# Performance work log

Measured on AMD Instinct MI355X. Metric: run time of the kernel, lower is better.

The kernel has to match this reference:

```python
import jax, jax.numpy as jnp
import numpy as np


def setup_inputs() -> dict:
    key = jax.random.key(0)
    k1, k2 = jax.random.split(key)
    B, F = 256, 512
    mu_in = jax.random.normal(k1, (B, F), dtype=jnp.float32)
    Sigma_in = jax.random.normal(k2, (B, F, F), dtype=jnp.float32)
    return {"mu_in": mu_in, "Sigma_in": Sigma_in}


def reference(mu_in, Sigma_in):
    # mu_out = softmax(mu_in, axis=1)
    p = jax.nn.softmax(mu_in, axis=1)  # [B, F]
    # Per-sample softmax Jacobian J = diag(p) - p p^T (closed form of the
    # autograd.functional.jacobian block-diagonal the torch code extracts).
    # Sigma_out = J @ Sigma_in @ J^T, computed without materializing J:
    #   (Sigma J^T)_ij = p_j * (Sigma_ij - (Sigma @ p)_i)
    Sp = jnp.einsum("bij,bj->bi", Sigma_in, p)  # [B, F]
    M = p[:, None, :] * (Sigma_in - Sp[:, :, None])  # Sigma @ J^T, [B, F, F]
    #   (J M)_ik = p_i * (M_ik - (p^T M)_k)
    pM = jnp.einsum("bi,bik->bk", p, M)  # [B, F]
    Sigma_out = p[:, :, None] * (M - pM[:, None, :])  # [B, F, F]
    return (p, Sigma_out)
```

## Files before the change

kernel.cpp:

```cpp
#include <hip/hip_runtime.h>

#define FDIM 512
#define S_ELEMS (FDIM * FDIM)

#define R_OFF      0
#define C_OFF      131072
#define S_OFF      262144
#define CP_OFF     262400
#define WS_FLOATS  (262400 + 256 * 8 * 512)

__device__ __forceinline__ float4 ld4(const float* p) { return *(const float4*)p; }

typedef float vf4 __attribute__((ext_vector_type(4)));
__device__ __forceinline__ void st4nt(float* p, float4 v) {
    __builtin_nontemporal_store(*(vf4*)&v, (vf4*)p);
}

__global__ __launch_bounds__(256)
void k1_rc(const float* __restrict__ mu,
           const float* __restrict__ Sigma,
           float* __restrict__ p_out,
           float* __restrict__ ws) {
    const int bid  = blockIdx.x;
    const int b    = bid >> 3;
    const int slab = bid & 7;
    const int t = threadIdx.x;
    const int w = t >> 6;
    const int l = t & 63;

    __shared__ __align__(16) float p_lds[FDIM];
    __shared__ __align__(16) float cred[4][FDIM];
    __shared__ float red[4];
    __shared__ float sc[1];

    const float x0 = mu[(size_t)b * FDIM + t];
    const float x1 = mu[(size_t)b * FDIM + t + 256];
    float m = fmaxf(x0, x1);
    #pragma unroll
    for (int off = 32; off >= 1; off >>= 1) m = fmaxf(m, __shfl_xor(m, off));
    if (l == 0) red[w] = m;
    __syncthreads();
    if (t == 0) sc[0] = fmaxf(fmaxf(red[0], red[1]), fmaxf(red[2], red[3]));
    __syncthreads();
    const float mx = sc[0];
    const float e0 = __expf(x0 - mx);
    const float e1 = __expf(x1 - mx);
    float ssum = e0 + e1;
    #pragma unroll
    for (int off = 32; off >= 1; off >>= 1) ssum += __shfl_xor(ssum, off);
    if (l == 0) red[w] = ssum;
    __syncthreads();
    if (t == 0) sc[0] = red[0] + red[1] + red[2] + red[3];
    __syncthreads();
    const float inv = 1.0f / sc[0];
    const float pva = e0 * inv, pvb = e1 * inv;
    p_lds[t] = pva;
    p_lds[t + 256] = pvb;
    if (slab == 0) {
        p_out[(size_t)b * FDIM + t] = pva;
        p_out[(size_t)b * FDIM + t + 256] = pvb;
    }
    __syncthreads();

    const float4 p0 = ld4(&p_lds[4 * l]);
    const float4 p1 = ld4(&p_lds[256 + 4 * l]);

    const int i0 = slab * 64 + w * 16;
    const float* base = Sigma + (size_t)b * S_ELEMS + (size_t)i0 * FDIM + 4 * l;
    float* r_ws = ws + R_OFF + (size_t)b * FDIM;

    float4 c0 = make_float4(0.f, 0.f, 0.f, 0.f);
    float4 c1 = make_float4(0.f, 0.f, 0.f, 0.f);
    float4 A0, A1, B0, B1, C0, C1, D0, D1;

#define LD1(P, q) do { const float* gp_ = base + (size_t)(q) * FDIM;        \
    P##0 = ld4(gp_); P##1 = ld4(gp_ + 256); } while (0)

#define RCROW(v0, v1, q) do {                                               \
    const int i_ = i0 + (q);                                                \
    float dot = v0.x*p0.x + v0.y*p0.y + v0.z*p0.z + v0.w*p0.w               \
              + v1.x*p1.x + v1.y*p1.y + v1.z*p1.z + v1.w*p1.w;              \
    _Pragma("unroll")                                                       \
    for (int o_ = 32; o_ >= 1; o_ >>= 1) dot += __shfl_xor(dot, o_);        \
    if (l == 0) r_ws[i_] = dot;                                             \
    const float pi_ = p_lds[i_];                                            \
    c0.x += pi_*v0.x; c0.y += pi_*v0.y; c0.z += pi_*v0.z; c0.w += pi_*v0.w; \
    c1.x += pi_*v1.x; c1.y += pi_*v1.y; c1.z += pi_*v1.z; c1.w += pi_*v1.w; \
} while (0)
#define RC1(P, q) RCROW(P##0, P##1, q)

    LD1(A, 0); LD1(B, 1); LD1(C, 2);
    RC1(A, 0);  LD1(D, 3);
    RC1(B, 1);  LD1(A, 4);
    RC1(C, 2);  LD1(B, 5);
    RC1(D, 3);  LD1(C, 6);
    RC1(A, 4);  LD1(D, 7);
    RC1(B, 5);  LD1(A, 8);
    RC1(C, 6);  LD1(B, 9);
    RC1(D, 7);  LD1(C, 10);
    RC1(A, 8);  LD1(D, 11);
    RC1(B, 9);  LD1(A, 12);
    RC1(C, 10); LD1(B, 13);
    RC1(D, 11); LD1(C, 14);
    RC1(A, 12); LD1(D, 15);
    RC1(B, 13);
    RC1(C, 14);
    RC1(D, 15);
#undef LD1
#undef RCROW
#undef RC1

    *(float4*)&cred[w][4 * l] = c0;
    *(float4*)&cred[w][256 + 4 * l] = c1;
    __syncthreads();
    const float ca = cred[0][t] + cred[1][t] + cred[2][t] + cred[3][t];
    const float cb = cred[0][t + 256] + cred[1][t + 256] + cred[2][t + 256] + cred[3][t + 256];
    float* cp = ws + CP_OFF + ((size_t)b * 8 + slab) * FDIM;
    cp[t] = ca;
    cp[t + 256] = cb;
}

__global__ __launch_bounds__(512)
void k2b_cs(const float* __restrict__ p_out, float* __restrict__ ws) {
    const int b = blockIdx.x;
    const int t = threadIdx.x;
    const int w = t >> 6;
    const int l = t & 63;
    __shared__ float red[8];

    float cc = 0.f;
    #pragma unroll
    for (int j = 0; j < 8; ++j)
        cc += ws[CP_OFF + ((size_t)b * 8 + j) * FDIM + t];
    ws[C_OFF + (size_t)b * FDIM + t] = cc;

    float sv = p_out[(size_t)b * FDIM + t] * ws[R_OFF + (size_t)b * FDIM + t];
    #pragma unroll
    for (int off = 32; off >= 1; off >>= 1) sv += __shfl_xor(sv, off);
    if (l == 0) red[w] = sv;
    __syncthreads();
    if (t == 0) {
        float tt = 0.f;
        for (int j = 0; j < 8; ++j) tt += red[j];
        ws[S_OFF + b] = tt;
    }
}

__global__ __launch_bounds__(256)
void k3_out(const float* __restrict__ Sigma,
            const float* __restrict__ p_out,
            const float* __restrict__ ws,
            float* __restrict__ S_out) {
    const int bid  = 2047 - (int)blockIdx.x;
    const int b    = bid >> 3;
    const int slab = bid & 7;
    const int t = threadIdx.x;
    const int w = t >> 6;
    const int l = t & 63;

    __shared__ float pr[64], rr[64];
    if (t < 64) {
        pr[t] = p_out[(size_t)b * FDIM + slab * 64 + t];
        rr[t] = ws[R_OFF + (size_t)b * FDIM + slab * 64 + t];
    }
    const float4 p0 = ld4(p_out + (size_t)b * FDIM + 4 * l);
    const float4 p1 = ld4(p_out + (size_t)b * FDIM + 256 + 4 * l);
    const float4 c0 = ld4(ws + C_OFF + (size_t)b * FDIM + 4 * l);
    const float4 c1 = ld4(ws + C_OFF + (size_t)b * FDIM + 256 + 4 * l);
    const float  s  = ws[S_OFF + b];
    __syncthreads();

    const int i0 = slab * 64 + w * 16;
    const float* base = Sigma + (size_t)b * S_ELEMS + (size_t)i0 * FDIM + 4 * l;
    float* obase      = S_out + (size_t)b * S_ELEMS + (size_t)i0 * FDIM + 4 * l;

    float4 A0, A1, B0, B1, C0, C1, D0, D1;

#define LD3(P, q) do { const float* gp_ = base + (size_t)(q) * FDIM;        \
    P##0 = ld4(gp_); P##1 = ld4(gp_ + 256); } while (0)

#define OWROW(v0, v1, q) do {                                               \
    const int lr_ = w * 16 + (q);                                           \
    const float pi_ = pr[lr_];                                              \
    const float f_  = s - rr[lr_];                                          \
    float4 o0, o1;                                                          \
    o0.x = pi_*p0.x*(v0.x + (f_ - c0.x));                                   \
    o0.y = pi_*p0.y*(v0.y + (f_ - c0.y));                                   \
    o0.z = pi_*p0.z*(v0.z + (f_ - c0.z));                                   \
    o0.w = pi_*p0.w*(v0.w + (f_ - c0.w));                                   \
    o1.x = pi_*p1.x*(v1.x + (f_ - c1.x));                                   \
    o1.y = pi_*p1.y*(v1.y + (f_ - c1.y));                                   \
    o1.z = pi_*p1.z*(v1.z + (f_ - c1.z));                                   \
    o1.w = pi_*p1.w*(v1.w + (f_ - c1.w));                                   \
    float* op_ = obase + (size_t)(q) * FDIM;                                \
    st4nt(op_, o0); st4nt(op_ + 256, o1);                                   \
} while (0)
#define OW3(P, q) OWROW(P##0, P##1, q)

    LD3(A, 0); LD3(B, 1); LD3(C, 2);
    OW3(A, 0);  LD3(D, 3);
    OW3(B, 1);  LD3(A, 4);
    OW3(C, 2);  LD3(B, 5);
    OW3(D, 3);  LD3(C, 6);
    OW3(A, 4);  LD3(D, 7);
    OW3(B, 5);  LD3(A, 8);
    OW3(C, 6);  LD3(B, 9);
    OW3(D, 7);  LD3(C, 10);
    OW3(A, 8);  LD3(D, 11);
    OW3(B, 9);  LD3(A, 12);
    OW3(C, 10); LD3(B, 13);
    OW3(D, 11); LD3(C, 14);
    OW3(A, 12); LD3(D, 15);
    OW3(B, 13);
    OW3(C, 14);
    OW3(D, 15);
#undef LD3
#undef OWROW
#undef OW3
}

__global__ __launch_bounds__(1024, 1)
void rvsoftmax_fused(const float* __restrict__ mu,
                     const float* __restrict__ Sigma,
                     float* __restrict__ p_out,
                     float* __restrict__ S_out) {
    const int b = blockIdx.x, t = threadIdx.x, w = t >> 6, l = t & 63;
    __shared__ __align__(16) float p_lds[FDIM];
    __shared__ __align__(16) float r_lds[FDIM];
    __shared__ __align__(16) float c_lds[FDIM];
    __shared__ __align__(16) float c_stage[16][FDIM];
    __shared__ float red[16]; __shared__ float sc[2];
    float x = (t < FDIM) ? mu[(size_t)b * FDIM + t] : -__builtin_inff();
    float m = x;
    #pragma unroll
    for (int off = 32; off >= 1; off >>= 1) m = fmaxf(m, __shfl_xor(m, off));
    if (l == 0) red[w] = m;
    __syncthreads();
    if (t == 0) { float mm = red[0]; for (int j = 1; j < 16; ++j) mm = fmaxf(mm, red[j]); sc[0] = mm; }
    __syncthreads();
    const float mx = sc[0];
    float e = (t < FDIM) ? __expf(x - mx) : 0.f;
    float ssum = e;
    #pragma unroll
    for (int off = 32; off >= 1; off >>= 1) ssum += __shfl_xor(ssum, off);
    if (l == 0) red[w] = ssum;
    __syncthreads();
    if (t == 0) { float tt = 0.f; for (int j = 0; j < 16; ++j) tt += red[j]; sc[0] = tt; }
    __syncthreads();
    const float inv = 1.0f / sc[0];
    if (t < FDIM) { float pv = e * inv; p_lds[t] = pv; p_out[(size_t)b * FDIM + t] = pv; }
    __syncthreads();
    const float* Sb = Sigma + (size_t)b * S_ELEMS;
    const float4 p0 = ld4(&p_lds[4 * l]);
    const float4 p1 = ld4(&p_lds[256 + 4 * l]);
    float4 c0 = make_float4(0.f, 0.f, 0.f, 0.f), c1 = make_float4(0.f, 0.f, 0.f, 0.f);
    for (int j = 0; j < 32; ++j) {
        const int i = j * 16 + w;
        const float* row = Sb + (size_t)i * FDIM;
        const float4 a0 = ld4(&row[4 * l]); const float4 a1 = ld4(&row[256 + 4 * l]);
        const float pi = p_lds[i];
        float dot = a0.x*p0.x + a0.y*p0.y + a0.z*p0.z + a0.w*p0.w
                  + a1.x*p1.x + a1.y*p1.y + a1.z*p1.z + a1.w*p1.w;
        #pragma unroll
        for (int off = 32; off >= 1; off >>= 1) dot += __shfl_xor(dot, off);
        if (l == 0) r_lds[i] = dot;
        c0.x += pi*a0.x; c0.y += pi*a0.y; c0.z += pi*a0.z; c0.w += pi*a0.w;
        c1.x += pi*a1.x; c1.y += pi*a1.y; c1.z += pi*a1.z; c1.w += pi*a1.w;
    }
    *(float4*)&c_stage[w][4 * l] = c0;
    *(float4*)&c_stage[w][256 + 4 * l] = c1;
    __syncthreads();
    if (t < FDIM) {
        float cc = 0.f;
        #pragma unroll
        for (int j = 0; j < 16; ++j) cc += c_stage[j][t];
        c_lds[t] = cc;
    }
    __syncthreads();
    float sv = (t < FDIM) ? p_lds[t] * r_lds[t] : 0.f;
    #pragma unroll
    for (int off = 32; off >= 1; off >>= 1) sv += __shfl_xor(sv, off);
    if (l == 0) red[w] = sv;
    __syncthreads();
    if (t == 0) { float tt = 0.f; for (int j = 0; j < 16; ++j) tt += red[j]; sc[1] = tt; }
    __syncthreads();
    const float s = sc[1];
    const float4 cc0 = ld4(&c_lds[4 * l]); const float4 cc1 = ld4(&c_lds[256 + 4 * l]);
    float* Ob = S_out + (size_t)b * S_ELEMS;
    for (int j = 31; j >= 0; --j) {
        const int i = j * 16 + w;
        const float* row = Sb + (size_t)i * FDIM;
        float* orow = Ob + (size_t)i * FDIM;
        const float4 a0 = ld4(&row[4 * l]); const float4 a1 = ld4(&row[256 + 4 * l]);
        const float pi = p_lds[i];
        const float f = s - r_lds[i];
        float4 o0, o1;
        o0.x = pi*p0.x*(a0.x + (f - cc0.x)); o0.y = pi*p0.y*(a0.y + (f - cc0.y));
        o0.z = pi*p0.z*(a0.z + (f - cc0.z)); o0.w = pi*p0.w*(a0.w + (f - cc0.w));
        o1.x = pi*p1.x*(a1.x + (f - cc1.x)); o1.y = pi*p1.y*(a1.y + (f - cc1.y));
        o1.z = pi*p1.z*(a1.z + (f - cc1.z)); o1.w = pi*p1.w*(a1.w + (f - cc1.w));
        *(float4*)&orow[4 * l] = o0;
        *(float4*)&orow[256 + 4 * l] = o1;
    }
}

extern "C" void kernel_launch(void* const* d_in, const int* in_sizes, int n_in,
                              void* d_out, int out_size, void* d_ws, size_t ws_size,
                              hipStream_t stream) {
    (void)in_sizes; (void)n_in; (void)out_size;
    const float* mu    = (const float*)d_in[0];
    const float* Sigma = (const float*)d_in[1];
    float* p_out = (float*)d_out;
    float* S_out = (float*)d_out + (size_t)256 * FDIM;

    if (ws_size >= (size_t)WS_FLOATS * sizeof(float)) {
        float* ws = (float*)d_ws;
        hipLaunchKernelGGL(k1_rc,   dim3(2048), dim3(256), 0, stream, mu, Sigma, p_out, ws);
        hipLaunchKernelGGL(k2b_cs,  dim3(256),  dim3(512), 0, stream, p_out, ws);
        hipLaunchKernelGGL(k3_out,  dim3(2048), dim3(256), 0, stream, Sigma, p_out, ws, S_out);
    } else {
        hipLaunchKernelGGL(rvsoftmax_fused, dim3(256), dim3(1024), 0, stream,
                           mu, Sigma, p_out, S_out);
    }
}
```

Measured before the change: 136.9 us.

## Split batch into groups so Sigma stays cache-resident between passes; fold reduction kernel

```diff
diff --git a/kernel.cpp b/kernel.cpp
--- a/kernel.cpp
+++ b/kernel.cpp
@@ -2,12 +2,13 @@
 
 #define FDIM 512
 #define S_ELEMS (FDIM * FDIM)
+#define NB 256
+#define GROUPS 4
+#define BPG (NB / GROUPS)
 
 #define R_OFF      0
-#define C_OFF      131072
-#define S_OFF      262144
-#define CP_OFF     262400
-#define WS_FLOATS  (262400 + 256 * 8 * 512)
+#define CP_OFF     (NB * FDIM)
+#define WS_FLOATS  (NB * FDIM + NB * 8 * FDIM)
 
 __device__ __forceinline__ float4 ld4(const float* p) { return *(const float4*)p; }
 
@@ -20,9 +21,10 @@
 void k1_rc(const float* __restrict__ mu,
            const float* __restrict__ Sigma,
            float* __restrict__ p_out,
-           float* __restrict__ ws) {
+           float* __restrict__ ws,
+           int b0) {
     const int bid  = blockIdx.x;
-    const int b    = bid >> 3;
+    const int b    = b0 + (bid >> 3);
     const int slab = bid & 7;
     const int t = threadIdx.x;
     const int w = t >> 6;
@@ -120,55 +122,23 @@
     cp[t + 256] = cb;
 }
 
-__global__ __launch_bounds__(512)
-void k2b_cs(const float* __restrict__ p_out, float* __restrict__ ws) {
-    const int b = blockIdx.x;
-    const int t = threadIdx.x;
-    const int w = t >> 6;
-    const int l = t & 63;
-    __shared__ float red[8];
-
-    float cc = 0.f;
-    #pragma unroll
-    for (int j = 0; j < 8; ++j)
-        cc += ws[CP_OFF + ((size_t)b * 8 + j) * FDIM + t];
-    ws[C_OFF + (size_t)b * FDIM + t] = cc;
-
-    float sv = p_out[(size_t)b * FDIM + t] * ws[R_OFF + (size_t)b * FDIM + t];
-    #pragma unroll
-    for (int off = 32; off >= 1; off >>= 1) sv += __shfl_xor(sv, off);
-    if (l == 0) red[w] = sv;
-    __syncthreads();
-    if (t == 0) {
-        float tt = 0.f;
-        for (int j = 0; j < 8; ++j) tt += red[j];
-        ws[S_OFF + b] = tt;
-    }
-}
-
 __global__ __launch_bounds__(256)
 void k3_out(const float* __restrict__ Sigma,
             const float* __restrict__ p_out,
             const float* __restrict__ ws,
-            float* __restrict__ S_out) {
-    const int bid  = 2047 - (int)blockIdx.x;
-    const int b    = bid >> 3;
+            float* __restrict__ S_out,
+            int b0) {
+    const int bid  = 511 - (int)blockIdx.x;
+    const int b    = b0 + (bid >> 3);
     const int slab = bid & 7;
     const int t = threadIdx.x;
     const int w = t >> 6;
     const int l = t & 63;
 
+    __shared__ __align__(16) float c_lds[FDIM];
     __shared__ float pr[64], rr[64];
-    if (t < 64) {
-        pr[t] = p_out[(size_t)b * FDIM + slab * 64 + t];
-        rr[t] = ws[R_OFF + (size_t)b * FDIM + slab * 64 + t];
-    }
-    const float4 p0 = ld4(p_out + (size_t)b * FDIM + 4 * l);
-    const float4 p1 = ld4(p_out + (size_t)b * FDIM + 256 + 4 * l);
-    const float4 c0 = ld4(ws + C_OFF + (size_t)b * FDIM + 4 * l);
-    const float4 c1 = ld4(ws + C_OFF + (size_t)b * FDIM + 256 + 4 * l);
-    const float  s  = ws[S_OFF + b];
-    __syncthreads();
+    __shared__ float red[4];
+    __shared__ float s_sh;
 
     const int i0 = slab * 64 + w * 16;
     const float* base = Sigma + (size_t)b * S_ELEMS + (size_t)i0 * FDIM + 4 * l;
@@ -178,6 +148,39 @@
 
 #define LD3(P, q) do { const float* gp_ = base + (size_t)(q) * FDIM;        \
     P##0 = ld4(gp_); P##1 = ld4(gp_ + 256); } while (0)
+
+    LD3(A, 0); LD3(B, 1); LD3(C, 2);
+
+    const float* cp = ws + CP_OFF + (size_t)b * 8 * FDIM;
+    float ca = 0.f, cb = 0.f;
+    #pragma unroll
+    for (int j = 0; j < 8; ++j) {
+        ca += cp[(size_t)j * FDIM + t];
+        cb += cp[(size_t)j * FDIM + t + 256];
+    }
+    c_lds[t] = ca;
+    c_lds[t + 256] = cb;
+
+    const float* pb_g = p_out + (size_t)b * FDIM;
+    const float* rb_g = ws + R_OFF + (size_t)b * FDIM;
+    const float pv0 = pb_g[t], pv1 = pb_g[t + 256];
+    const float rv0 = rb_g[t], rv1 = rb_g[t + 256];
+    float sv = pv0 * rv0 + pv1 * rv1;
+    #pragma unroll
+    for (int off = 32; off >= 1; off >>= 1) sv += __shfl_xor(sv, off);
+    if (l == 0) red[w] = sv;
+    if (t < 64) {
+        pr[t] = pb_g[slab * 64 + t];
+        rr[t] = rb_g[slab * 64 + t];
+    }
+    __syncthreads();
+    if (t == 0) s_sh = red[0] + red[1] + red[2] + red[3];
+    __syncthreads();
+    const float s = s_sh;
+    const float4 p0 = ld4(pb_g + 4 * l);
+    const float4 p1 = ld4(pb_g + 256 + 4 * l);
+    const float4 c0 = ld4(&c_lds[4 * l]);
+    const float4 c1 = ld4(&c_lds[256 + 4 * l]);
 
 #define OWROW(v0, v1, q) do {                                               \
     const int lr_ = w * 16 + (q);                                           \
@@ -197,7 +200,6 @@
 } while (0)
 #define OW3(P, q) OWROW(P##0, P##1, q)
 
-    LD3(A, 0); LD3(B, 1); LD3(C, 2);
     OW3(A, 0);  LD3(D, 3);
     OW3(B, 1);  LD3(A, 4);
     OW3(C, 2);  LD3(B, 5);
@@ -311,15 +313,18 @@
     const float* mu    = (const float*)d_in[0];
     const float* Sigma = (const float*)d_in[1];
     float* p_out = (float*)d_out;
-    float* S_out = (float*)d_out + (size_t)256 * FDIM;
+    float* S_out = (float*)d_out + (size_t)NB * FDIM;
 
     if (ws_size >= (size_t)WS_FLOATS * sizeof(float)) {
         float* ws = (float*)d_ws;
-        hipLaunchKernelGGL(k1_rc,   dim3(2048), dim3(256), 0, stream, mu, Sigma, p_out, ws);
-        hipLaunchKernelGGL(k2b_cs,  dim3(256),  dim3(512), 0, stream, p_out, ws);
-        hipLaunchKernelGGL(k3_out,  dim3(2048), dim3(256), 0, stream, Sigma, p_out, ws, S_out);
+        for (int g = 0; g < GROUPS; ++g) {
+            hipLaunchKernelGGL(k1_rc,  dim3(BPG * 8), dim3(256), 0, stream,
+                               mu, Sigma, p_out, ws, g * BPG);
+            hipLaunchKernelGGL(k3_out, dim3(BPG * 8), dim3(256), 0, stream,
+                               Sigma, p_out, ws, S_out, g * BPG);
+        }
     } else {
-        hipLaunchKernelGGL(rvsoftmax_fused, dim3(256), dim3(1024), 0, stream,
+        hipLaunchKernelGGL(rvsoftmax_fused, dim3(NB), dim3(1024), 0, stream,
                            mu, Sigma, p_out, S_out);
     }
 }
```

Result: slower. 149.9 us (+9.4%).

## Split batch into groups for cache reuse of Sigma between passes

Applied to the files above, without the earlier changes.

```diff
diff --git a/kernel.cpp b/kernel.cpp
--- a/kernel.cpp
+++ b/kernel.cpp
@@ -2,12 +2,17 @@
 
 #define FDIM 512
 #define S_ELEMS (FDIM * FDIM)
-
-#define R_OFF      0
-#define C_OFF      131072
-#define S_OFF      262144
-#define CP_OFF     262400
-#define WS_FLOATS  (262400 + 256 * 8 * 512)
+#define NB 256
+#define GROUPS 2
+#define BPG (NB / GROUPS)
+#define SLABS 16
+#define GBLK (BPG * SLABS)
+
+#define R_OFF  0
+#define C_OFF  (NB * FDIM)
+#define S_OFF  (2 * NB * FDIM)
+#define CP_OFF (2 * NB * FDIM + NB)
+#define WS_FLOATS (CP_OFF + NB * SLABS * FDIM)
 
 __device__ __forceinline__ float4 ld4(const float* p) { return *(const float4*)p; }
 
@@ -17,13 +22,14 @@
 }
 
 __global__ __launch_bounds__(256)
-void k1_rc(const float* __restrict__ mu,
-           const float* __restrict__ Sigma,
-           float* __restrict__ p_out,
-           float* __restrict__ ws) {
+void k1_kernel(const float* __restrict__ mu,
+               const float* __restrict__ Sigma,
+               float* __restrict__ p_out,
+               float* __restrict__ ws,
+               int b0) {
     const int bid  = blockIdx.x;
-    const int b    = bid >> 3;
-    const int slab = bid & 7;
+    const int b    = b0 + (bid >> 4);
+    const int slab = bid & 15;
     const int t = threadIdx.x;
     const int w = t >> 6;
     const int l = t & 63;
@@ -31,7 +37,7 @@
     __shared__ __align__(16) float p_lds[FDIM];
     __shared__ __align__(16) float cred[4][FDIM];
     __shared__ float red[4];
-    __shared__ float sc[1];
+    __shared__ float sc1;
 
     const float x0 = mu[(size_t)b * FDIM + t];
     const float x1 = mu[(size_t)b * FDIM + t + 256];
@@ -40,9 +46,9 @@
     for (int off = 32; off >= 1; off >>= 1) m = fmaxf(m, __shfl_xor(m, off));
     if (l == 0) red[w] = m;
     __syncthreads();
-    if (t == 0) sc[0] = fmaxf(fmaxf(red[0], red[1]), fmaxf(red[2], red[3]));
-    __syncthreads();
-    const float mx = sc[0];
+    if (t == 0) sc1 = fmaxf(fmaxf(red[0], red[1]), fmaxf(red[2], red[3]));
+    __syncthreads();
+    const float mx = sc1;
     const float e0 = __expf(x0 - mx);
     const float e1 = __expf(x1 - mx);
     float ssum = e0 + e1;
@@ -50,9 +56,9 @@
     for (int off = 32; off >= 1; off >>= 1) ssum += __shfl_xor(ssum, off);
     if (l == 0) red[w] = ssum;
     __syncthreads();
-    if (t == 0) sc[0] = red[0] + red[1] + red[2] + red[3];
-    __syncthreads();
-    const float inv = 1.0f / sc[0];
+    if (t == 0) sc1 = red[0] + red[1] + red[2] + red[3];
+    __syncthreads();
+    const float inv = 1.0f / sc1;
     const float pva = e0 * inv, pvb = e1 * inv;
     p_lds[t] = pva;
     p_lds[t + 256] = pvb;
@@ -65,7 +71,7 @@
     const float4 p0 = ld4(&p_lds[4 * l]);
     const float4 p1 = ld4(&p_lds[256 + 4 * l]);
 
-    const int i0 = slab * 64 + w * 16;
+    const int i0 = slab * 32 + w * 8;
     const float* base = Sigma + (size_t)b * S_ELEMS + (size_t)i0 * FDIM + 4 * l;
     float* r_ws = ws + R_OFF + (size_t)b * FDIM;
 
@@ -90,22 +96,14 @@
 #define RC1(P, q) RCROW(P##0, P##1, q)
 
     LD1(A, 0); LD1(B, 1); LD1(C, 2);
-    RC1(A, 0);  LD1(D, 3);
-    RC1(B, 1);  LD1(A, 4);
-    RC1(C, 2);  LD1(B, 5);
-    RC1(D, 3);  LD1(C, 6);
-    RC1(A, 4);  LD1(D, 7);
-    RC1(B, 5);  LD1(A, 8);
-    RC1(C, 6);  LD1(B, 9);
-    RC1(D, 7);  LD1(C, 10);
-    RC1(A, 8);  LD1(D, 11);
-    RC1(B, 9);  LD1(A, 12);
-    RC1(C, 10); LD1(B, 13);
-    RC1(D, 11); LD1(C, 14);
-    RC1(A, 12); LD1(D, 15);
-    RC1(B, 13);
-    RC1(C, 14);
-    RC1(D, 15);
+    RC1(A, 0); LD1(D, 3);
+    RC1(B, 1); LD1(A, 4);
+    RC1(C, 2); LD1(B, 5);
+    RC1(D, 3); LD1(C, 6);
+    RC1(A, 4); LD1(D, 7);
+    RC1(B, 5);
+    RC1(C, 6);
+    RC1(D, 7);
 #undef LD1
 #undef RCROW
 #undef RC1
@@ -115,14 +113,14 @@
     __syncthreads();
     const float ca = cred[0][t] + cred[1][t] + cred[2][t] + cred[3][t];
     const float cb = cred[0][t + 256] + cred[1][t + 256] + cred[2][t + 256] + cred[3][t + 256];
-    float* cp = ws + CP_OFF + ((size_t)b * 8 + slab) * FDIM;
+    float* cp = ws + CP_OFF + ((size_t)b * SLABS + slab) * FDIM;
     cp[t] = ca;
     cp[t + 256] = cb;
 }
 
 __global__ __launch_bounds__(512)
-void k2b_cs(const float* __restrict__ p_out, float* __restrict__ ws) {
-    const int b = blockIdx.x;
+void k2b_kernel(const float* __restrict__ p_out, float* __restrict__ ws, int b0) {
+    const int b = b0 + (int)blockIdx.x;
     const int t = threadIdx.x;
     const int w = t >> 6;
     const int l = t & 63;
@@ -130,8 +128,8 @@
 
     float cc = 0.f;
     #pragma unroll
-    for (int j = 0; j < 8; ++j)
-        cc += ws[CP_OFF + ((size_t)b * 8 + j) * FDIM + t];
+    for (int j = 0; j < SLABS; ++j)
+        cc += ws[CP_OFF + ((size_t)b * SLABS + j) * FDIM + t];
     ws[C_OFF + (size_t)b * FDIM + t] = cc;
 
     float sv = p_out[(size_t)b * FDIM + t] * ws[R_OFF + (size_t)b * FDIM + t];
@@ -147,40 +145,46 @@
 }
 
 __global__ __launch_bounds__(256)
-void k3_out(const float* __restrict__ Sigma,
-            const float* __restrict__ p_out,
-            const float* __restrict__ ws,
-            float* __restrict__ S_out) {
-    const int bid  = 2047 - (int)blockIdx.x;
-    const int b    = bid >> 3;
-    const int slab = bid & 7;
+void k3_kernel(const float* __restrict__ Sigma,
+               const float* __restrict__ p_out,
+               const float* __restrict__ ws,
+               float* __restrict__ S_out,
+               int b0) {
+    const int bid  = (int)gridDim.x - 1 - (int)blockIdx.x;
+    const int b    = b0 + (bid >> 4);
+    const int slab = bid & 15;
     const int t = threadIdx.x;
     const int w = t >> 6;
     const int l = t & 63;
 
-    __shared__ float pr[64], rr[64];
-    if (t < 64) {
-        pr[t] = p_out[(size_t)b * FDIM + slab * 64 + t];
-        rr[t] = ws[R_OFF + (size_t)b * FDIM + slab * 64 + t];
-    }
-    const float4 p0 = ld4(p_out + (size_t)b * FDIM + 4 * l);
-    const float4 p1 = ld4(p_out + (size_t)b * FDIM + 256 + 4 * l);
+    __shared__ float pr[32], rr[32];
+
+    const int i0 = slab * 32 + w * 8;
+    const float* base = Sigma + (size_t)b * S_ELEMS + (size_t)i0 * FDIM + 4 * l;
+    float* obase      = S_out + (size_t)b * S_ELEMS + (size_t)i0 * FDIM + 4 * l;
+
+    float4 A0, A1, B0, B1, C0, C1, D0, D1;
+
+#define LD3(P, q) do { const float* gp_ = base + (size_t)(q) * FDIM;        \
+    P##0 = ld4(gp_); P##1 = ld4(gp_ + 256); } while (0)
+
+    LD3(A, 0); LD3(B, 1); LD3(C, 2);
+
+    const float* pb_g = p_out + (size_t)b * FDIM;
+    const float* rb_g = ws + R_OFF + (size_t)b * FDIM;
+    if (t < 32) {
+        pr[t] = pb_g[slab * 32 + t];
+        rr[t] = rb_g[slab * 32 + t];
+    }
+    const float  s  = ws[S_OFF + b];
+    const float4 p0 = ld4(pb_g + 4 * l);
+    const float4 p1 = ld4(pb_g + 256 + 4 * l);
     const float4 c0 = ld4(ws + C_OFF + (size_t)b * FDIM + 4 * l);
     const float4 c1 = ld4(ws + C_OFF + (size_t)b * FDIM + 256 + 4 * l);
-    const float  s  = ws[S_OFF + b];
-    __syncthreads();
-
-    const int i0 = slab * 64 + w * 16;
-    const float* base = Sigma + (size_t)b * S_ELEMS + (size_t)i0 * FDIM + 4 * l;
-    float* obase      = S_out + (size_t)b * S_ELEMS + (size_t)i0 * FDIM + 4 * l;
-
-    float4 A0, A1, B0, B1, C0, C1, D0, D1;
-
-#define LD3(P, q) do { const float* gp_ = base + (size_t)(q) * FDIM;        \
-    P##0 = ld4(gp_); P##1 = ld4(gp_ + 256); } while (0)
+    __syncthreads();
 
 #define OWROW(v0, v1, q) do {                                               \
-    const int lr_ = w * 16 + (q);                                           \
+    const int lr_ = w * 8 + (q);                                            \
     const float pi_ = pr[lr_];                                              \
     const float f_  = s - rr[lr_];                                          \
     float4 o0, o1;                                                          \
@@ -197,23 +201,14 @@
 } while (0)
 #define OW3(P, q) OWROW(P##0, P##1, q)
 
-    LD3(A, 0); LD3(B, 1); LD3(C, 2);
-    OW3(A, 0);  LD3(D, 3);
-    OW3(B, 1);  LD3(A, 4);
-    OW3(C, 2);  LD3(B, 5);
-    OW3(D, 3);  LD3(C, 6);
-    OW3(A, 4);  LD3(D, 7);
-    OW3(B, 5);  LD3(A, 8);
-    OW3(C, 6);  LD3(B, 9);
-    OW3(D, 7);  LD3(C, 10);
-    OW3(A, 8);  LD3(D, 11);
-    OW3(B, 9);  LD3(A, 12);
-    OW3(C, 10); LD3(B, 13);
-    OW3(D, 11); LD3(C, 14);
-    OW3(A, 12); LD3(D, 15);
-    OW3(B, 13);
-    OW3(C, 14);
-    OW3(D, 15);
+    OW3(A, 0); LD3(D, 3);
+    OW3(B, 1); LD3(A, 4);
+    OW3(C, 2); LD3(B, 5);
+    OW3(D, 3); LD3(C, 6);
+    OW3(A, 4); LD3(D, 7);
+    OW3(B, 5);
+    OW3(C, 6);
+    OW3(D, 7);
 #undef LD3
 #undef OWROW
 #undef OW3
@@ -311,15 +306,21 @@
     const float* mu    = (const float*)d_in[0];
     const float* Sigma = (const float*)d_in[1];
     float* p_out = (float*)d_out;
-    float* S_out = (float*)d_out + (size_t)256 * FDIM;
+    float* S_out = (float*)d_out + (size_t)NB * FDIM;
 
     if (ws_size >= (size_t)WS_FLOATS * sizeof(float)) {
         float* ws = (float*)d_ws;
-        hipLaunchKernelGGL(k1_rc,   dim3(2048), dim3(256), 0, stream, mu, Sigma, p_out, ws);
-        hipLaunchKernelGGL(k2b_cs,  dim3(256),  dim3(512), 0, stream, p_out, ws);
-        hipLaunchKernelGGL(k3_out,  dim3(2048), dim3(256), 0, stream, Sigma, p_out, ws, S_out);
+        for (int g = 0; g < GROUPS; ++g) {
+            const int b0 = g * BPG;
+            hipLaunchKernelGGL(k1_kernel,  dim3(GBLK), dim3(256), 0, stream,
+                               mu, Sigma, p_out, ws, b0);
+            hipLaunchKernelGGL(k2b_kernel, dim3(BPG),  dim3(512), 0, stream,
+                               p_out, ws, b0);
+            hipLaunchKernelGGL(k3_kernel,  dim3(GBLK), dim3(256), 0, stream,
+                               Sigma, p_out, ws, S_out, b0);
+        }
     } else {
-        hipLaunchKernelGGL(rvsoftmax_fused, dim3(256), dim3(1024), 0, stream,
+        hipLaunchKernelGGL(rvsoftmax_fused, dim3(NB), dim3(1024), 0, stream,
                            mu, Sigma, p_out, S_out);
     }
 }
```

Measured after the change: 144.6 us. +5.6%, slower.

## Cache Sigma as fp16 in workspace during first pass and read it in output pass

Applied to the files above, without the earlier changes.

```diff
diff --git a/kernel.cpp b/kernel.cpp
--- a/kernel.cpp
+++ b/kernel.cpp
@@ -1,26 +1,43 @@
 #include <hip/hip_runtime.h>
+#include <hip/hip_fp16.h>
 
 #define FDIM 512
 #define S_ELEMS (FDIM * FDIM)
-
-#define R_OFF      0
-#define C_OFF      131072
-#define S_OFF      262144
-#define CP_OFF     262400
-#define WS_FLOATS  (262400 + 256 * 8 * 512)
+#define NB 256
+#define SLABS 8
+#define NBLK (NB * SLABS)
+
+#define R_OFF  0
+#define C_OFF  131072
+#define S_OFF  262144
+#define CP_OFF 262400
+#define H_OFF  (CP_OFF + NB * SLABS * FDIM)
+#define WS_FLOATS (H_OFF + NB * S_ELEMS / 2)
 
 __device__ __forceinline__ float4 ld4(const float* p) { return *(const float4*)p; }
 
 typedef float vf4 __attribute__((ext_vector_type(4)));
+__device__ __forceinline__ float4 ld4nt(const float* p) {
+    vf4 v = __builtin_nontemporal_load((const vf4*)p);
+    return *(float4*)&v;
+}
 __device__ __forceinline__ void st4nt(float* p, float4 v) {
     __builtin_nontemporal_store(*(vf4*)&v, (vf4*)p);
 }
+__device__ __forceinline__ unsigned pk2(float a, float b) {
+    __half2 h = __floats2half2_rn(a, b);
+    return *reinterpret_cast<unsigned*>(&h);
+}
+__device__ __forceinline__ float2 uh2(unsigned u) {
+    __half2 h = *reinterpret_cast<__half2*>(&u);
+    return __half22float2(h);
+}
 
 __global__ __launch_bounds__(256)
-void k1_rc(const float* __restrict__ mu,
-           const float* __restrict__ Sigma,
-           float* __restrict__ p_out,
-           float* __restrict__ ws) {
+void k1_kernel(const float* __restrict__ mu,
+               const float* __restrict__ Sigma,
+               float* __restrict__ p_out,
+               float* __restrict__ ws) {
     const int bid  = blockIdx.x;
     const int b    = bid >> 3;
     const int slab = bid & 7;
@@ -31,7 +48,7 @@
     __shared__ __align__(16) float p_lds[FDIM];
     __shared__ __align__(16) float cred[4][FDIM];
     __shared__ float red[4];
-    __shared__ float sc[1];
+    __shared__ float sc1;
 
     const float x0 = mu[(size_t)b * FDIM + t];
     const float x1 = mu[(size_t)b * FDIM + t + 256];
@@ -40,9 +57,9 @@
     for (int off = 32; off >= 1; off >>= 1) m = fmaxf(m, __shfl_xor(m, off));
     if (l == 0) red[w] = m;
     __syncthreads();
-    if (t == 0) sc[0] = fmaxf(fmaxf(red[0], red[1]), fmaxf(red[2], red[3]));
-    __syncthreads();
-    const float mx = sc[0];
+    if (t == 0) sc1 = fmaxf(fmaxf(red[0], red[1]), fmaxf(red[2], red[3]));
+    __syncthreads();
+    const float mx = sc1;
     const float e0 = __expf(x0 - mx);
     const float e1 = __expf(x1 - mx);
     float ssum = e0 + e1;
@@ -50,9 +67,9 @@
     for (int off = 32; off >= 1; off >>= 1) ssum += __shfl_xor(ssum, off);
     if (l == 0) red[w] = ssum;
     __syncthreads();
-    if (t == 0) sc[0] = red[0] + red[1] + red[2] + red[3];
-    __syncthreads();
-    const float inv = 1.0f / sc[0];
+    if (t == 0) sc1 = red[0] + red[1] + red[2] + red[3];
+    __syncthreads();
+    const float inv = 1.0f / sc1;
     const float pva = e0 * inv, pvb = e1 * inv;
     p_lds[t] = pva;
     p_lds[t + 256] = pvb;
@@ -68,13 +85,15 @@
     const int i0 = slab * 64 + w * 16;
     const float* base = Sigma + (size_t)b * S_ELEMS + (size_t)i0 * FDIM + 4 * l;
     float* r_ws = ws + R_OFF + (size_t)b * FDIM;
+    __half* h_base = (__half*)(ws + H_OFF) + (size_t)b * S_ELEMS
+                   + (size_t)i0 * FDIM + 8 * l;
 
     float4 c0 = make_float4(0.f, 0.f, 0.f, 0.f);
     float4 c1 = make_float4(0.f, 0.f, 0.f, 0.f);
     float4 A0, A1, B0, B1, C0, C1, D0, D1;
 
 #define LD1(P, q) do { const float* gp_ = base + (size_t)(q) * FDIM;        \
-    P##0 = ld4(gp_); P##1 = ld4(gp_ + 256); } while (0)
+    P##0 = ld4nt(gp_); P##1 = ld4nt(gp_ + 256); } while (0)
 
 #define RCROW(v0, v1, q) do {                                               \
     const int i_ = i0 + (q);                                                \
@@ -86,6 +105,10 @@
     const float pi_ = p_lds[i_];                                            \
     c0.x += pi_*v0.x; c0.y += pi_*v0.y; c0.z += pi_*v0.z; c0.w += pi_*v0.w; \
     c1.x += pi_*v1.x; c1.y += pi_*v1.y; c1.z += pi_*v1.z; c1.w += pi_*v1.w; \
+    uint4 hu_;                                                              \
+    hu_.x = pk2(v0.x, v0.y); hu_.y = pk2(v0.z, v0.w);                       \
+    hu_.z = pk2(v1.x, v1.y); hu_.w = pk2(v1.z, v1.w);                       \
+    *(uint4*)(h_base + (size_t)(q) * FDIM) = hu_;                           \
 } while (0)
 #define RC1(P, q) RCROW(P##0, P##1, q)
 
@@ -115,13 +138,13 @@
     __syncthreads();
     const float ca = cred[0][t] + cred[1][t] + cred[2][t] + cred[3][t];
     const float cb = cred[0][t + 256] + cred[1][t + 256] + cred[2][t + 256] + cred[3][t + 256];
-    float* cp = ws + CP_OFF + ((size_t)b * 8 + slab) * FDIM;
+    float* cp = ws + CP_OFF + ((size_t)b * SLABS + slab) * FDIM;
     cp[t] = ca;
     cp[t + 256] = cb;
 }
 
 __global__ __launch_bounds__(512)
-void k2b_cs(const float* __restrict__ p_out, float* __restrict__ ws) {
+void k2b_kernel(const float* __restrict__ p_out, float* __restrict__ ws) {
     const int b = blockIdx.x;
     const int t = threadIdx.x;
     const int w = t >> 6;
@@ -130,8 +153,8 @@
 
     float cc = 0.f;
     #pragma unroll
-    for (int j = 0; j < 8; ++j)
-        cc += ws[CP_OFF + ((size_t)b * 8 + j) * FDIM + t];
+    for (int j = 0; j < SLABS; ++j)
+        cc += ws[CP_OFF + ((size_t)b * SLABS + j) * FDIM + t];
     ws[C_OFF + (size_t)b * FDIM + t] = cc;
 
     float sv = p_out[(size_t)b * FDIM + t] * ws[R_OFF + (size_t)b * FDIM + t];
@@ -147,11 +170,10 @@
 }
 
 __global__ __launch_bounds__(256)
-void k3_out(const float* __restrict__ Sigma,
-            const float* __restrict__ p_out,
-            const float* __restrict__ ws,
-            float* __restrict__ S_out) {
-    const int bid  = 2047 - (int)blockIdx.x;
+void k3_kernel(const float* __restrict__ p_out,
+               const float* __restrict__ ws,
+               float* __restrict__ S_out) {
+    const int bid  = NBLK - 1 - (int)blockIdx.x;
     const int b    = bid >> 3;
     const int slab = bid & 7;
     const int t = threadIdx.x;
@@ -159,64 +181,68 @@
     const int l = t & 63;
 
     __shared__ float pr[64], rr[64];
+
+    const int i0 = slab * 64 + w * 16;
+    const __half* hb = (const __half*)(ws + H_OFF) + (size_t)b * S_ELEMS
+                     + (size_t)i0 * FDIM + 8 * l;
+    float* obase = S_out + (size_t)b * S_ELEMS + (size_t)i0 * FDIM + 4 * l;
+
+    uint4 UA, UB, UC, UD;
+
+#define LD3(U, q) U = *(const uint4*)(hb + (size_t)(q) * FDIM)
+
+    LD3(UA, 0); LD3(UB, 1); LD3(UC, 2);
+
+    const float* pb_g = p_out + (size_t)b * FDIM;
+    const float* rb_g = ws + R_OFF + (size_t)b * FDIM;
     if (t < 64) {
-        pr[t] = p_out[(size_t)b * FDIM + slab * 64 + t];
-        rr[t] = ws[R_OFF + (size_t)b * FDIM + slab * 64 + t];
-    }
-    const float4 p0 = ld4(p_out + (size_t)b * FDIM + 4 * l);
-    const float4 p1 = ld4(p_out + (size_t)b * FDIM + 256 + 4 * l);
+        pr[t] = pb_g[slab * 64 + t];
+        rr[t] = rb_g[slab * 64 + t];
+    }
+    const float  s  = ws[S_OFF + b];
+    const float4 p0 = ld4(pb_g + 4 * l);
+    const float4 p1 = ld4(pb_g + 256 + 4 * l);
     const float4 c0 = ld4(ws + C_OFF + (size_t)b * FDIM + 4 * l);
     const float4 c1 = ld4(ws + C_OFF + (size_t)b * FDIM + 256 + 4 * l);
-    const float  s  = ws[S_OFF + b];
-    __syncthreads();
-
-    const int i0 = slab * 64 + w * 16;
-    const float* base = Sigma + (size_t)b * S_ELEMS + (size_t)i0 * FDIM + 4 * l;
-    float* obase      = S_out + (size_t)b * S_ELEMS + (size_t)i0 * FDIM + 4 * l;
-
-    float4 A0, A1, B0, B1, C0, C1, D0, D1;
-
-#define LD3(P, q) do { const float* gp_ = base + (size_t)(q) * FDIM;        \
-    P##0 = ld4(gp_); P##1 = ld4(gp_ + 256); } while (0)
-
-#define OWROW(v0, v1, q) do {                                               \
+    __syncthreads();
+
+#define OWROW(U, q) do {                                                    \
+    const float2 f0_ = uh2(U.x), f1_ = uh2(U.y);                            \
+    const float2 f2_ = uh2(U.z), f3_ = uh2(U.w);                            \
     const int lr_ = w * 16 + (q);                                           \
     const float pi_ = pr[lr_];                                              \
     const float f_  = s - rr[lr_];                                          \
     float4 o0, o1;                                                          \
-    o0.x = pi_*p0.x*(v0.x + (f_ - c0.x));                                   \
-    o0.y = pi_*p0.y*(v0.y + (f_ - c0.y));                                   \
-    o0.z = pi_*p0.z*(v0.z + (f_ - c0.z));                                   \
-    o0.w = pi_*p0.w*(v0.w + (f_ - c0.w));                                   \
-    o1.x = pi_*p1.x*(v1.x + (f_ - c1.x));                                   \
-    o1.y = pi_*p1.y*(v1.y + (f_ - c1.y));                                   \
-    o1.z = pi_*p1.z*(v1.z + (f_ - c1.z));                                   \
-    o1.w = pi_*p1.w*(v1.w + (f_ - c1.w));                                   \
+    o0.x = pi_*p0.x*(f0_.x + (f_ - c0.x));                                  \
+    o0.y = pi_*p0.y*(f0_.y + (f_ - c0.y));                                  \
+    o0.z = pi_*p0.z*(f1_.x + (f_ - c0.z));                                  \
+    o0.w = pi_*p0.w*(f1_.y + (f_ - c0.w));                                  \
+    o1.x = pi_*p1.x*(f2_.x + (f_ - c1.x));                                  \
+    o1.y = pi_*p1.y*(f2_.y + (f_ - c1.y));                                  \
+    o1.z = pi_*p1.z*(f3_.x + (f_ - c1.z));                                  \
+    o1.w = pi_*p1.w*(f3_.y + (f_ - c1.w));                                  \
     float* op_ = obase + (size_t)(q) * FDIM;                                \
     st4nt(op_, o0); st4nt(op_ + 256, o1);                                   \
 } while (0)
-#define OW3(P, q) OWROW(P##0, P##1, q)
-
-    LD3(A, 0); LD3(B, 1); LD3(C, 2);
-    OW3(A, 0);  LD3(D, 3);
-    OW3(B, 1);  LD3(A, 4);
-    OW3(C, 2);  LD3(B, 5);
-    OW3(D, 3);  LD3(C, 6);
-    OW3(A, 4);  LD3(D, 7);
-    OW3(B, 5);  LD3(A, 8);
-    OW3(C, 6);  LD3(B, 9);
-    OW3(D, 7);  LD3(C, 10);
-    OW3(A, 8);  LD3(D, 11);
-    OW3(B, 9);  LD3(A, 12);
-    OW3(C, 10); LD3(B, 13);
-    OW3(D, 11); LD3(C, 14);
-    OW3(A, 12); LD3(D, 15);
-    OW3(B, 13);
-    OW3(C, 14);
-    OW3(D, 15);
+
+    OWROW(UA, 0);  LD3(UD, 3);
+    OWROW(UB, 1);  LD3(UA, 4);
+    OWROW(UC, 2);  LD3(UB, 5);
+    OWROW(UD, 3);  LD3(UC, 6);
+    OWROW(UA, 4);  LD3(UD, 7);
+    OWROW(UB, 5);  LD3(UA, 8);
+    OWROW(UC, 6);  LD3(UB, 9);
+    OWROW(UD, 7);  LD3(UC, 10);
+    OWROW(UA, 8);  LD3(UD, 11);
+    OWROW(UB, 9);  LD3(UA, 12);
+    OWROW(UC, 10); LD3(UB, 13);
+    OWROW(UD, 11); LD3(UC, 14);
+    OWROW(UA, 12); LD3(UD, 15);
+    OWROW(UB, 13);
+    OWROW(UC, 14);
+    OWROW(UD, 15);
 #undef LD3
 #undef OWROW
-#undef OW3
 }
 
 __global__ __launch_bounds__(1024, 1)
@@ -311,15 +337,18 @@
     const float* mu    = (const float*)d_in[0];
     const float* Sigma = (const float*)d_in[1];
     float* p_out = (float*)d_out;
-    float* S_out = (float*)d_out + (size_t)256 * FDIM;
+    float* S_out = (float*)d_out + (size_t)NB * FDIM;
 
     if (ws_size >= (size_t)WS_FLOATS * sizeof(float)) {
         float* ws = (float*)d_ws;
-        hipLaunchKernelGGL(k1_rc,   dim3(2048), dim3(256), 0, stream, mu, Sigma, p_out, ws);
-        hipLaunchKernelGGL(k2b_cs,  dim3(256),  dim3(512), 0, stream, p_out, ws);
-        hipLaunchKernelGGL(k3_out,  dim3(2048), dim3(256), 0, stream, Sigma, p_out, ws, S_out);
+        hipLaunchKernelGGL(k1_kernel,  dim3(NBLK), dim3(256), 0, stream,
+                           mu, Sigma, p_out, ws);
+        hipLaunchKernelGGL(k2b_kernel, dim3(NB),   dim3(512), 0, stream,
+                           p_out, ws);
+        hipLaunchKernelGGL(k3_kernel,  dim3(NBLK), dim3(256), 0, stream,
+                           p_out, ws, S_out);
     } else {
-        hipLaunchKernelGGL(rvsoftmax_fused, dim3(256), dim3(1024), 0, stream,
+        hipLaunchKernelGGL(rvsoftmax_fused, dim3(NB), dim3(1024), 0, stream,
                            mu, Sigma, p_out, S_out);
     }
 }
```

Result: faster. 134.1 us (-2.1%).
